# Performance work log

Measured on AMD Instinct MI355X. Metric: run time of the kernel, lower is better.

## Reference

```python
import jax, jax.numpy as jnp
import numpy as np

EPS = 1e-7

# ---- Poincare ball (c=1) manifold ops ----

def _logmap0(y):
    n = jnp.linalg.norm(y, axis=-1, keepdims=True)
    n = jnp.clip(n, EPS, 1.0 - 1e-5)
    return jnp.arctanh(n) * y / n


def _expmap0(v):
    n = jnp.maximum(jnp.linalg.norm(v, axis=-1, keepdims=True), EPS)
    return jnp.tanh(n) * v / n


def _pair_dist(q):
    # q: [B,N,H,D] points in the Poincare ball.
    # d(x,y) = arccosh(1 + 2||x-y||^2 / ((1-||x||^2)(1-||y||^2)))  (== 2 artanh ||(-x)+_m y||)
    sq = jnp.sum(q * q, axis=-1)                       # [B,N,H]
    dot = jnp.einsum('bnhd,bmhd->bnmh', q, q)          # [B,N,N,H] (batched GEMM)
    diff = jnp.maximum(sq[:, :, None, :] + sq[:, None, :, :] - 2.0 * dot, 0.0)
    denom = jnp.maximum((1.0 - sq[:, :, None, :]) * (1.0 - sq[:, None, :, :]), EPS)
    return jnp.arccosh(jnp.maximum(1.0 + 2.0 * diff / denom, 1.0 + EPS))  # [B,N,N,H]


def _hgat(x, adj, W, a_src, a_dst, multihead):
    # Hyperbolic GAT layer: log-map to tangent at origin, per-head linear +
    # masked GAT attention, exp-map back. use_act=False, no bias.
    xt = _logmap0(x)                                   # [B,N,Din]
    h = jnp.einsum('bnd,hde->bnhe', xt, W)             # [B,N,H,D]
    es = jnp.einsum('bnhe,he->bnh', h, a_src)
    ed = jnp.einsum('bnhe,he->bnh', h, a_dst)
    e = jax.nn.leaky_relu(es[:, :, None, :] + ed[:, None, :, :], 0.2)  # [B,N,N,H]
    e = jnp.where(adj[:, :, :, None] > 0, e, -1e9)
    att = jax.nn.softmax(e, axis=2)                    # over neighbors
    out = jnp.einsum('bnmh,bmhe->bnhe', att, h)        # [B,N,H,D]
    if multihead:
        return _expmap0(out)                           # per-head hyperbolic points
    B, N, H, D = out.shape
    return _expmap0(out.reshape(B, N, H * D))          # concat heads


def setup_inputs() -> dict:
    key = jax.random.key(0)
    B, N, DIN, DATT, DOUT, H = 8, 1024, 256, 64, 256, 4
    ks = jax.random.split(key, 8)
    x = _expmap0(0.5 * jax.random.normal(ks[0], (B, N, DIN), dtype=jnp.float32))
    a0 = (jax.random.uniform(ks[1], (B, N, N)) < 0.05).astype(jnp.float32)
    adj = jnp.maximum(a0, jnp.swapaxes(a0, -1, -2))
    adj = jnp.maximum(adj, jnp.eye(N, dtype=jnp.float32)[None])
    flags = jnp.ones((B, N), dtype=jnp.float32)
    s_in = 1.0 / np.sqrt(DIN)
    Wq = jax.random.normal(ks[2], (H, DIN, DATT), dtype=jnp.float32) * s_in
    aq_src = jax.random.normal(ks[3], (H, DATT), dtype=jnp.float32) / np.sqrt(DATT)
    aq_dst = jax.random.normal(ks[4], (H, DATT), dtype=jnp.float32) / np.sqrt(DATT)
    Dv = DOUT // H
    Wv = jax.random.normal(ks[5], (H, DIN, Dv), dtype=jnp.float32) * s_in
    av_src = jax.random.normal(ks[6], (H, Dv), dtype=jnp.float32) / np.sqrt(Dv)
    av_dst = jax.random.normal(ks[7], (H, Dv), dtype=jnp.float32) / np.sqrt(Dv)
    r = jnp.ones((H,), dtype=jnp.float32) * 5.0
    t = jnp.ones((H,), dtype=jnp.float32)
    return {"x": x, "adj": adj, "flags": flags, "Wq": Wq, "aq_src": aq_src,
            "aq_dst": aq_dst, "Wv": Wv, "av_src": av_src, "av_dst": av_dst,
            "r": r, "t": t}


def reference(x, adj, flags, Wq, aq_src, aq_dst, Wv, av_src, av_dst, r, t):
    B, N = adj.shape[0], adj.shape[1]
    query = _hgat(x, adj, Wq, aq_src, aq_dst, True)    # [B,N,H,DATT]
    value = _hgat(x, adj, Wv, av_src, av_dst, False)   # [B,N,DOUT]
    dist = _pair_dist(query)                           # [B,N,N,H]
    dist = dist.reshape(-1, B, N, N)                   # faithful torch .view(-1,*adj.shape)
    att = jnp.tanh((r[:, None, None, None] - dist) * t[:, None, None, None])
    att = att.reshape(-1, B, N, N).mean(axis=0)        # head-average -> [B,N,N]
    att = (att + jnp.swapaxes(att, -1, -2)) / 2.0      # symmetrize
    return value, att
```

## Files before the change

### kernel.cpp

```cpp
#include <hip/hip_runtime.h>
#include <hip/hip_bf16.h>
#include <math.h>

#define DEV __device__ __forceinline__

constexpr int B = 8, N = 1024, DIN = 256, H = 4, DATT = 64, DV = 64;
constexpr int BN = B * N;
constexpr int HD = H * DATT;
constexpr int HDV = H * DV;
constexpr int COLS = HD + HDV;
constexpr int BHN = B * H * N;
constexpr float EPSF = 1e-7f;

using short8 = __attribute__((ext_vector_type(8))) short;
using f32x4  = __attribute__((ext_vector_type(4))) float;

DEV unsigned short f2bf(float f) {
    __hip_bfloat16 h = __float2bfloat16(f);
    return *reinterpret_cast<unsigned short*>(&h);
}
DEV float bfu2f(unsigned short u) { return __uint_as_float(((unsigned)u) << 16); }

__global__ void k_scale(const float* __restrict__ x, float* __restrict__ s) {
    int p = blockIdx.x * 4 + (threadIdx.x >> 6);
    int l = threadIdx.x & 63;
    const float4* xr = reinterpret_cast<const float4*>(x + (size_t)p * DIN);
    float4 u = xr[l];
    float ss = u.x * u.x + u.y * u.y + u.z * u.z + u.w * u.w;
    for (int m = 32; m; m >>= 1) ss += __shfl_xor(ss, m);
    if (l == 0) {
        float n = sqrtf(ss);
        n = fminf(fmaxf(n, EPSF), 1.0f - 1e-5f);
        float at = 0.5f * __logf((1.f + n) / (1.f - n));
        s[p] = at / n;
    }
}

__global__ void k_wcat(const float* __restrict__ Wq, const float* __restrict__ Wv,
                       float* __restrict__ Wc) {
    int idx = blockIdx.x * 256 + threadIdx.x;
    int k = idx >> 9, c = idx & 511;
    int cc = c & 255;
    int h = cc >> 6, e = cc & 63;
    const float* src = (c < HD) ? Wq : Wv;
    Wc[idx] = src[(h * DIN + k) * 64 + e];
}

__global__ __launch_bounds__(256) void k_gemm(const float* __restrict__ x,
                                              const float* __restrict__ s,
                                              const float* __restrict__ Wc,
                                              float* __restrict__ hall) {
    __shared__ float As[16][68];
    __shared__ float Bs[16][68];
    int bm = blockIdx.x, bn = blockIdx.y;
    int tid = threadIdx.x;
    int ty = tid >> 4, tx = tid & 15;
    float acc[4][4] = {};
    int rowbase = bm * 64, colbase = bn * 64;
    int am = tid >> 2;
    int ak = (tid & 3) * 4;
    float sc = s[rowbase + am];
    for (int kt = 0; kt < DIN; kt += 16) {
        float4 u = *reinterpret_cast<const float4*>(x + (size_t)(rowbase + am) * DIN + kt + ak);
        As[ak + 0][am] = u.x * sc;
        As[ak + 1][am] = u.y * sc;
        As[ak + 2][am] = u.z * sc;
        As[ak + 3][am] = u.w * sc;
        int bk = tid >> 4, bc = (tid & 15) * 4;
        float4 w4 = *reinterpret_cast<const float4*>(Wc + (size_t)(kt + bk) * COLS + colbase + bc);
        *reinterpret_cast<float4*>(&Bs[bk][bc]) = w4;
        __syncthreads();
        for (int k = 0; k < 16; k++) {
            float4 a4 = *reinterpret_cast<const float4*>(&As[k][ty * 4]);
            float4 b4 = *reinterpret_cast<const float4*>(&Bs[k][tx * 4]);
            float av[4] = {a4.x, a4.y, a4.z, a4.w};
            float bv[4] = {b4.x, b4.y, b4.z, b4.w};
            for (int i = 0; i < 4; i++)
                for (int j = 0; j < 4; j++) acc[i][j] = fmaf(av[i], bv[j], acc[i][j]);
        }
        __syncthreads();
    }
    for (int i = 0; i < 4; i++) {
        float4 o = make_float4(acc[i][0], acc[i][1], acc[i][2], acc[i][3]);
        *reinterpret_cast<float4*>(hall + (size_t)(rowbase + ty * 4 + i) * COLS + colbase + tx * 4) = o;
    }
}

__global__ __launch_bounds__(256) void k_hT(const float* __restrict__ hall,
                                            unsigned short* __restrict__ hallT) {
    int jt = blockIdx.x, h = blockIdx.y, b = blockIdx.z;
    __shared__ float T[64][69];
    int t = threadIdx.x;
    int bh = b * H + h;
    int jl = t >> 2, cg = t & 3;
    int el = t >> 2, seg = t & 3;
    #pragma unroll
    for (int pass = 0; pass < 2; pass++) {
        int colbase = (pass == 0) ? h * 64 : 256 + h * 64;
        __syncthreads();
        {
            const float* src = hall + (size_t)(b * N + jt * 64 + jl) * COLS + colbase + cg * 16;
            #pragma unroll
            for (int u = 0; u < 4; u++) {
                float4 v = *reinterpret_cast<const float4*>(src + u * 4);
                T[jl][cg * 16 + u * 4 + 0] = v.x;
                T[jl][cg * 16 + u * 4 + 1] = v.y;
                T[jl][cg * 16 + u * 4 + 2] = v.z;
                T[jl][cg * 16 + u * 4 + 3] = v.w;
            }
        }
        __syncthreads();
        {
            unsigned int pk[8];
            #pragma unroll
            for (int k = 0; k < 8; k++) {
                float f0 = T[seg * 16 + 2 * k][el];
                float f1 = T[seg * 16 + 2 * k + 1][el];
                pk[k] = (unsigned)f2bf(f0) | ((unsigned)f2bf(f1) << 16);
            }
            unsigned short* dst = hallT + ((size_t)(bh * 128 + pass * 64 + el)) * 1024
                                  + jt * 64 + seg * 16;
            *reinterpret_cast<uint4*>(dst)     = make_uint4(pk[0], pk[1], pk[2], pk[3]);
            *reinterpret_cast<uint4*>(dst + 8) = make_uint4(pk[4], pk[5], pk[6], pk[7]);
        }
    }
}

__global__ void k_esed(const float* __restrict__ hall, const float* __restrict__ aqs,
                       const float* __restrict__ aqd, const float* __restrict__ avs,
                       const float* __restrict__ avd, float* __restrict__ esq,
                       float* __restrict__ edq, float* __restrict__ esv,
                       float* __restrict__ edv) {
    int p = blockIdx.x;
    int h = threadIdx.x >> 6, e = threadIdx.x & 63;
    float hq = hall[(size_t)p * COLS + h * 64 + e];
    float hv = hall[(size_t)p * COLS + 256 + h * 64 + e];
    float v1 = hq * aqs[h * 64 + e];
    float v2 = hq * aqd[h * 64 + e];
    float v3 = hv * avs[h * 64 + e];
    float v4 = hv * avd[h * 64 + e];
    for (int m = 32; m; m >>= 1) {
        v1 += __shfl_xor(v1, m); v2 += __shfl_xor(v2, m);
        v3 += __shfl_xor(v3, m); v4 += __shfl_xor(v4, m);
    }
    if (e == 0) {
        int b = p >> 10, n = p & 1023;
        int o = (b * H + h) * N + n;
        esq[o] = v1; edq[o] = v2; esv[o] = v3; edv[o] = v4;
    }
}

__global__ void k_stats(const float* __restrict__ adj, const float* __restrict__ esq,
                        const float* __restrict__ edq, const float* __restrict__ esv,
                        const float* __restrict__ edv, float* __restrict__ stats) {
    int bid = blockIdx.x;
    int i = bid & 1023;
    int bh = bid >> 10;
    int b = bh >> 2;
    int t = threadIdx.x;
    float esqi = esq[bid], esvi = esv[bid];
    const float* arow = adj + (size_t)(b * N + i) * N + t * 8;
    const float* edqr = edq + (size_t)bh * N + t * 8;
    const float* edvr = edv + (size_t)bh * N + t * 8;
    float4 a0 = *reinterpret_cast<const float4*>(arow);
    float4 a1 = *reinterpret_cast<const float4*>(arow + 4);
    float am[8] = {a0.x, a0.y, a0.z, a0.w, a1.x, a1.y, a1.z, a1.w};
    float4 q0 = *reinterpret_cast<const float4*>(edqr);
    float4 q1 = *reinterpret_cast<const float4*>(edqr + 4);
    float4 w0 = *reinterpret_cast<const float4*>(edvr);
    float4 w1 = *reinterpret_cast<const float4*>(edvr + 4);
    float edqv[8] = {q0.x, q0.y, q0.z, q0.w, q1.x, q1.y, q1.z, q1.w};
    float edvv[8] = {w0.x, w0.y, w0.z, w0.w, w1.x, w1.y, w1.z, w1.w};
    float eq[8], ev[8];
    float mq = -1e30f, mv = -1e30f;
    for (int j = 0; j < 8; j++) {
        bool msk = am[j] > 0.f;
        float q = esqi + edqv[j]; q = fmaxf(q, 0.2f * q);
        float v = esvi + edvv[j]; v = fmaxf(v, 0.2f * v);
        eq[j] = msk ? q : -1e30f;
        ev[j] = msk ? v : -1e30f;
        mq = fmaxf(mq, eq[j]); mv = fmaxf(mv, ev[j]);
    }
    __shared__ float red[2][2];
    __shared__ float red2[2][2];
    for (int m = 32; m; m >>= 1) { mq = fmaxf(mq, __shfl_xor(mq, m)); mv = fmaxf(mv, __shfl_xor(mv, m)); }
    int w = t >> 6;
    if ((t & 63) == 0) { red[w][0] = mq; red[w][1] = mv; }
    __syncthreads();
    mq = fmaxf(red[0][0], red[1][0]);
    mv = fmaxf(red[0][1], red[1][1]);
    float sq_ = 0.f, sv_ = 0.f;
    for (int j = 0; j < 8; j++) { sq_ += __expf(eq[j] - mq); sv_ += __expf(ev[j] - mv); }
    for (int m = 32; m; m >>= 1) { sq_ += __shfl_xor(sq_, m); sv_ += __shfl_xor(sv_, m); }
    if ((t & 63) == 0) { red2[w][0] = sq_; red2[w][1] = sv_; }
    __syncthreads();
    if (t == 0) {
        stats[bid] = mq;
        stats[BHN + bid] = red2[0][0] + red2[1][0];
        stats[2 * BHN + bid] = mv;
        stats[3 * BHN + bid] = red2[0][1] + red2[1][1];
    }
}

__global__ __launch_bounds__(512) void k_aggr(const float* __restrict__ adj,
        const unsigned short* __restrict__ hallT, const float* __restrict__ esq,
        const float* __restrict__ edq, const float* __restrict__ esv,
        const float* __restrict__ edv, const float* __restrict__ stats,
        float* __restrict__ outq, float* __restrict__ outv) {
    int f = blockIdx.x;
    int g = ((f & 7) << 7) | (f >> 3);
    int it = g & 31;
    int bh = g >> 5;
    int h = bh & 3, b = bh >> 2;
    int i0 = it * 32;
    int t = threadIdx.x;
    int lane = t & 63, wv = t >> 6;
    int team = wv >> 1;
    int mh = wv & 1;

    int i = i0 + mh * 16 + (lane & 15);
    int bi = bh * N + i;
    float esq_i = esq[bi], esv_i = esv[bi];
    float mq_i = stats[bi];           float isq_i = 1.f / stats[BHN + bi];
    float mv_i = stats[2 * BHN + bi]; float isv_i = 1.f / stats[3 * BHN + bi];
    const float* adjrow = adj + (size_t)(b * N + i) * N;
    const float* edqrow = edq + (size_t)bh * N;
    const float* edvrow = edv + (size_t)bh * N;
    int klo = lane >> 4;
    const unsigned short* bbq = hallT
        + ((size_t)(bh * 128 + (lane & 15))) * 1024 + klo * 8;
    const unsigned short* bbv = bbq + (size_t)64 * 1024;

    f32x4 accq[4] = {}, accv[4] = {};
    int jbase = team * 256;
    for (int jj = 0; jj < 8; jj++) {
        int j0 = jbase + jj * 32;
        float4 a0 = *reinterpret_cast<const float4*>(adjrow + j0 + klo * 8);
        float4 a1 = *reinterpret_cast<const float4*>(adjrow + j0 + klo * 8 + 4);
        float4 q0 = *reinterpret_cast<const float4*>(edqrow + j0 + klo * 8);
        float4 q1 = *reinterpret_cast<const float4*>(edqrow + j0 + klo * 8 + 4);
        float4 v0 = *reinterpret_cast<const float4*>(edvrow + j0 + klo * 8);
        float4 v1 = *reinterpret_cast<const float4*>(edvrow + j0 + klo * 8 + 4);
        float av[8] = {a0.x, a0.y, a0.z, a0.w, a1.x, a1.y, a1.z, a1.w};
        float eq[8] = {q0.x, q0.y, q0.z, q0.w, q1.x, q1.y, q1.z, q1.w};
        float ev[8] = {v0.x, v0.y, v0.z, v0.w, v1.x, v1.y, v1.z, v1.w};
        short8 afq, afv;
        #pragma unroll
        for (int u = 0; u < 8; u++) {
            bool on = av[u] > 0.f;
            float q = esq_i + eq[u]; q = fmaxf(q, 0.2f * q);
            float v = esv_i + ev[u]; v = fmaxf(v, 0.2f * v);
            float wq = on ? __expf(q - mq_i) * isq_i : 0.f;
            float wvv = on ? __expf(v - mv_i) * isv_i : 0.f;
            afq[u] = (short)f2bf(wq);
            afv[u] = (short)f2bf(wvv);
        }
        #pragma unroll
        for (int nt = 0; nt < 4; nt++) {
            short8 bq = *reinterpret_cast<const short8*>(bbq + j0 + nt * 16384);
            accq[nt] = __builtin_amdgcn_mfma_f32_16x16x32_bf16(afq, bq, accq[nt], 0, 0, 0);
            short8 bv = *reinterpret_cast<const short8*>(bbv + j0 + nt * 16384);
            accv[nt] = __builtin_amdgcn_mfma_f32_16x16x32_bf16(afv, bv, accv[nt], 0, 0, 0);
        }
    }

    __shared__ __align__(16) float red[8192];
    int slot = (team >> 1) * 2 + mh;
    float* buf = red + slot * 2048;
    __syncthreads();
    if (team & 1) {
        #pragma unroll
        for (int k = 0; k < 4; k++) {
            *reinterpret_cast<f32x4*>(&buf[(k * 64 + lane) * 4])       = accq[k];
            *reinterpret_cast<f32x4*>(&buf[((k + 4) * 64 + lane) * 4]) = accv[k];
        }
    }
    __syncthreads();
    if (!(team & 1)) {
        #pragma unroll
        for (int k = 0; k < 4; k++) {
            f32x4 pq = *reinterpret_cast<const f32x4*>(&buf[(k * 64 + lane) * 4]);
            f32x4 pv = *reinterpret_cast<const f32x4*>(&buf[((k + 4) * 64 + lane) * 4]);
            accq[k] += pq; accv[k] += pv;
        }
    }
    __syncthreads();
    if (team == 2) {
        float* d2 = red + mh * 2048;
        #pragma unroll
        for (int k = 0; k < 4; k++) {
            *reinterpret_cast<f32x4*>(&d2[(k * 64 + lane) * 4])       = accq[k];
            *reinterpret_cast<f32x4*>(&d2[((k + 4) * 64 + lane) * 4]) = accv[k];
        }
    }
    __syncthreads();
    if (team == 0) {
        float* s2 = red + mh * 2048;
        #pragma unroll
        for (int nt = 0; nt < 4; nt++) {
            f32x4 pq = *reinterpret_cast<const f32x4*>(&s2[(nt * 64 + lane) * 4]);
            f32x4 pv = *reinterpret_cast<const f32x4*>(&s2[((nt + 4) * 64 + lane) * 4]);
            #pragma unroll
            for (int r = 0; r < 4; r++) {
                int irow = i0 + mh * 16 + (lane >> 4) * 4 + r;
                int e = nt * 16 + (lane & 15);
                outq[(size_t)(b * N + irow) * 256 + h * 64 + e] = accq[nt][r] + pq[r];
                outv[(size_t)(b * N + irow) * 256 + h * 64 + e] = accv[nt][r] + pv[r];
            }
        }
    }
}

__global__ void k_expmap(const float* __restrict__ outq, const float* __restrict__ outv,
                         float* __restrict__ query, float* __restrict__ sq,
                         float* __restrict__ val) {
    int p = blockIdx.x, t = threadIdx.x;
    int h = t >> 6, e = t & 63;
    float v = outq[(size_t)p * HD + t];
    float ss = v * v;
    for (int m = 32; m; m >>= 1) ss += __shfl_xor(ss, m);
    float n = fmaxf(sqrtf(ss), EPSF);
    float tn = tanhf(n);
    query[(size_t)p * HD + t] = v * (tn / n);
    if (e == 0) sq[h * BN + p] = tn * tn;

    float vv = outv[(size_t)p * HDV + t];
    float s2 = vv * vv;
    for (int m = 32; m; m >>= 1) s2 += __shfl_xor(s2, m);
    __shared__ float part[4];
    if (e == 0) part[h] = s2;
    __syncthreads();
    float tot = part[0] + part[1] + part[2] + part[3];
    float nv = fmaxf(sqrtf(tot), EPSF);
    float sclv = tanhf(nv) / nv;
    val[(size_t)p * HDV + t] = vv * sclv;
}

DEV int swzX(int row, int ch) { return row * 64 + ((ch ^ (row & 7)) * 8); }

DEV void tsplit(float v, short& hs, short& ls) {
    unsigned vu = __float_as_uint(v);
    float lo = v - __uint_as_float(vu & 0xFFFF0000u);
    hs = (short)(unsigned short)(vu >> 16);
    ls = (short)(unsigned short)(__float_as_uint(lo) >> 16);
}

__global__ __launch_bounds__(256, 3) void k_att(const float* __restrict__ query,
        const float* __restrict__ sq, const float* __restrict__ rr,
        const float* __restrict__ tt, float* __restrict__ m_out) {
    int kc = blockIdx.x >> 1, xh = blockIdx.x & 1;
    int c = blockIdx.y >> 2, h = blockIdx.y & 3;
    int b2 = blockIdx.z;
    int t = threadIdx.x;
    int l = t & 63, w = t >> 6;

    __shared__ __align__(16) unsigned short Xh[64 * 64], Xl[64 * 64];
    __shared__ __align__(16) unsigned short Yh[128 * 64], Yl[128 * 64];
    __shared__ float sqX[64], sqY[128], isX[64], isY[128];

    int nstart = (b2 * 256 + kc * 64) & 1023;
    int mstart = c * 256 + xh * 128;

    int rowX = t >> 2, pX = t & 3;
    int rowY = t >> 1, pY = t & 1;

    float tacc[8][4] = {};

    #pragma unroll
    for (int a = 0; a < 4; a++) {
        int b = 2 * a + (b2 >> 2);
        __syncthreads();
        {
            const float4* sx4 = reinterpret_cast<const float4*>(
                query + (size_t)(b * N + nstart + rowX) * HD + h * 64);
            #pragma unroll
            for (int cch = 0; cch < 2; cch++) {
                short8 hx, lx;
                float4 v0 = sx4[pX * 4 + cch * 2];
                float4 v1 = sx4[pX * 4 + cch * 2 + 1];
                float vv[8] = {v0.x, v0.y, v0.z, v0.w, v1.x, v1.y, v1.z, v1.w};
                #pragma unroll
                for (int q = 0; q < 8; q++) { short hs, ls; tsplit(vv[q], hs, ls); hx[q] = hs; lx[q] = ls; }
                int idx = swzX(rowX, pX * 2 + cch);
                *reinterpret_cast<short8*>(&Xh[idx]) = hx;
                *reinterpret_cast<short8*>(&Xl[idx]) = lx;
            }
        }
        {
            const float4* sy4 = reinterpret_cast<const float4*>(
                query + (size_t)(b * N + mstart + rowY) * HD + h * 64);
            #pragma unroll
            for (int cch = 0; cch < 4; cch++) {
                short8 hy, ly;
                float4 v0 = sy4[pY * 8 + cch * 2];
                float4 v1 = sy4[pY * 8 + cch * 2 + 1];
                float vv[8] = {v0.x, v0.y, v0.z, v0.w, v1.x, v1.y, v1.z, v1.w};
                #pragma unroll
                for (int q = 0; q < 8; q++) { short hs, ls; tsplit(vv[q], hs, ls); hy[q] = hs; ly[q] = ls; }
                int idy = swzX(rowY, pY * 4 + cch);
                *reinterpret_cast<short8*>(&Yh[idy]) = hy;
                *reinterpret_cast<short8*>(&Yl[idy]) = ly;
            }
        }
        if (t < 64)  { float s = sq[h * BN + b * N + nstart + t]; sqX[t] = s; isX[t] = __builtin_amdgcn_rcpf(1.f - s); }
        else if (t < 192) { int tt2 = t - 64; float s = sq[h * BN + b * N + mstart + tt2]; sqY[tt2] = s; isY[tt2] = __builtin_amdgcn_rcpf(1.f - s); }
        __syncthreads();

        short8 Ah[2], Al[2];
        #pragma unroll
        for (int kk = 0; kk < 2; kk++) {
            int rx = w * 16 + (l & 15);
            int idx = swzX(rx, kk * 4 + (l >> 4));
            Ah[kk] = *reinterpret_cast<const short8*>(&Xh[idx]);
            Al[kk] = *reinterpret_cast<const short8*>(&Xl[idx]);
        }
        float ra = rr[a], ta = tt[a];
        float c1 = 2.f * ta;
        float c0 = c1 * ra * 1.44269504f;
        float sxr[4], ixr[4];
        #pragma unroll
        for (int r = 0; r < 4; r++) {
            int rx = w * 16 + (l >> 4) * 4 + r;
            sxr[r] = sqX[rx];
            ixr[r] = 2.f * isX[rx];
        }
        #pragma unroll
        for (int nt = 0; nt < 8; nt++) {
            int ry = nt * 16 + (l & 15);
            f32x4 acc = {};
            #pragma unroll
            for (int kk = 0; kk < 2; kk++) {
                int idy = swzX(ry, kk * 4 + (l >> 4));
                short8 Bh = *reinterpret_cast<const short8*>(&Yh[idy]);
                short8 Bl = *reinterpret_cast<const short8*>(&Yl[idy]);
                acc = __builtin_amdgcn_mfma_f32_16x16x32_bf16(Ah[kk], Bh, acc, 0, 0, 0);
                acc = __builtin_amdgcn_mfma_f32_16x16x32_bf16(Ah[kk], Bl, acc, 0, 0, 0);
                acc = __builtin_amdgcn_mfma_f32_16x16x32_bf16(Al[kk], Bh, acc, 0, 0, 0);
            }
            float sy = sqY[ry];
            float iy = isY[ry];
            #pragma unroll
            for (int r = 0; r < 4; r++) {
                float diff = fmaxf(fmaf(-2.f, acc[r], sxr[r] + sy), 0.f);
                float ixy = fminf(ixr[r] * iy, 2e7f);
                float z = fmaxf(fmaf(diff, ixy, 1.f), 1.f + EPSF);
                float s_ = z + __builtin_amdgcn_sqrtf(fmaf(z, z, -1.f));
                float l2 = __builtin_amdgcn_logf(s_);
                float ex = __builtin_amdgcn_exp2f(fmaf(-c1, l2, c0));
                float rc = __builtin_amdgcn_rcpf(ex + 1.f);
                tacc[nt][r] += fmaf(-2.f, rc, 1.f);
            }
        }
    }
    #pragma unroll
    for (int nt = 0; nt < 8; nt++) {
        #pragma unroll
        for (int r = 0; r < 4; r++) {
            int n_local = w * 16 + (l >> 4) * 4 + r;
            int n2 = c + 4 * (kc * 64 + n_local);
            int mloc = xh * 128 + nt * 16 + (l & 15);
            int m2 = 4 * mloc + h;
            m_out[((size_t)b2 << 20) + ((size_t)n2 << 10) + m2] = 0.25f * tacc[nt][r];
        }
    }
}

__global__ void k_sym(float* __restrict__ m) {
    int ti = blockIdx.x, tj = blockIdx.y, b = blockIdx.z;
    if (ti > tj) return;
    __shared__ float A[32][33], Bt[32][33];
    int t = threadIdx.x;
    int r = t >> 3, c4 = (t & 7) * 4;
    size_t baseA = ((size_t)b << 20) + (size_t)(ti * 32) * N + tj * 32;
    size_t baseB = ((size_t)b << 20) + (size_t)(tj * 32) * N + ti * 32;
    float4 ua = *reinterpret_cast<const float4*>(m + baseA + (size_t)r * N + c4);
    float4 ub = *reinterpret_cast<const float4*>(m + baseB + (size_t)r * N + c4);
    A[r][c4 + 0] = ua.x; A[r][c4 + 1] = ua.y; A[r][c4 + 2] = ua.z; A[r][c4 + 3] = ua.w;
    Bt[r][c4 + 0] = ub.x; Bt[r][c4 + 1] = ub.y; Bt[r][c4 + 2] = ub.z; Bt[r][c4 + 3] = ub.w;
    __syncthreads();
    for (int u = 0; u < 4; u++) {
        int cc = c4 + u;
        float oa = 0.5f * (A[r][cc] + Bt[cc][r]);
        float ob = 0.5f * (Bt[r][cc] + A[cc][r]);
        m[baseA + (size_t)r * N + cc] = oa;
        m[baseB + (size_t)r * N + cc] = ob;
    }
}

extern "C" void kernel_launch(void* const* d_in, const int* in_sizes, int n_in,
                              void* d_out, int out_size, void* d_ws, size_t ws_size,
                              hipStream_t stream) {
    const float* x   = (const float*)d_in[0];
    const float* adj = (const float*)d_in[1];
    const float* Wq  = (const float*)d_in[3];
    const float* aqs = (const float*)d_in[4];
    const float* aqd = (const float*)d_in[5];
    const float* Wv  = (const float*)d_in[6];
    const float* avs = (const float*)d_in[7];
    const float* avd = (const float*)d_in[8];
    const float* rr  = (const float*)d_in[9];
    const float* tt  = (const float*)d_in[10];

    float* ws = (float*)d_ws;
    float* s     = ws;
    float* Wc    = s + BN;
    float* hall  = Wc + 256 * COLS;
    float* esq   = hall + (size_t)BN * COLS;
    float* edq   = esq + BHN;
    float* esv   = edq + BHN;
    float* edv   = esv + BHN;
    float* stats = edv + BHN;
    float* outq  = stats + 4 * BHN;
    float* outv  = outq + (size_t)BN * HD;
    float* query = outq;
    float* sq    = outv + (size_t)BN * HDV;
    unsigned short* hallT = (unsigned short*)(sq + H * BN);
    size_t need = (size_t)((char*)(hallT + (size_t)BN * COLS) - (char*)ws);
    if (ws_size < need) return;

    float* val  = (float*)d_out;
    float* matt = (float*)d_out + (size_t)BN * HDV;

    k_scale<<<BN / 4, 256, 0, stream>>>(x, s);
    k_wcat<<<(256 * COLS) / 256, 256, 0, stream>>>(Wq, Wv, Wc);
    k_gemm<<<dim3(BN / 64, COLS / 64), 256, 0, stream>>>(x, s, Wc, hall);
    k_hT<<<dim3(16, H, B), 256, 0, stream>>>(hall, hallT);
    k_esed<<<BN, 256, 0, stream>>>(hall, aqs, aqd, avs, avd, esq, edq, esv, edv);
    k_stats<<<BHN, 128, 0, stream>>>(adj, esq, edq, esv, edv, stats);
    k_aggr<<<1024, 512, 0, stream>>>(adj, hallT, esq, edq, esv, edv, stats, outq, outv);
    k_expmap<<<BN, 256, 0, stream>>>(outq, outv, query, sq, val);
    k_att<<<dim3(8, 16, 8), 256, 0, stream>>>(query, sq, rr, tt, matt);
    k_sym<<<dim3(32, 32, 8), 256, 0, stream>>>(matt);
}
```

Measured before the change: 265.5 us.

## Precompute bf16 hi/lo query split in expmap and load MFMA operands from global

k_expmap now writes the query as precomputed bf16 high/low halves plus the reciprocal 1/(1-|q|^2), reusing the hall workspace. k_att drops its shared-memory staging, per-tile splitting and barriers, and instead loads MFMA operand fragments and the norm terms straight from global memory (relying on L1/L2). Its grid is flattened to 1D with a remapped block order to improve cache locality, and the occupancy hint is removed. This cuts LDS traffic, sync and redundant conversion work, but it adds uncoalesced, repeated global loads inside the inner loop.

```diff
diff --git a/kernel.cpp b/kernel.cpp
--- a/kernel.cpp
+++ b/kernel.cpp
@@ -20,6 +20,13 @@
     return *reinterpret_cast<unsigned short*>(&h);
 }
 DEV float bfu2f(unsigned short u) { return __uint_as_float(((unsigned)u) << 16); }
+
+DEV void tsplit(float v, short& hs, short& ls) {
+    unsigned vu = __float_as_uint(v);
+    float lo = v - __uint_as_float(vu & 0xFFFF0000u);
+    hs = (short)(unsigned short)(vu >> 16);
+    ls = (short)(unsigned short)(__float_as_uint(lo) >> 16);
+}
 
 __global__ void k_scale(const float* __restrict__ x, float* __restrict__ s) {
     int p = blockIdx.x * 4 + (threadIdx.x >> 6);
@@ -312,7 +319,8 @@
 }
 
 __global__ void k_expmap(const float* __restrict__ outq, const float* __restrict__ outv,
-                         float* __restrict__ query, float* __restrict__ sq,
+                         unsigned short* __restrict__ qh, unsigned short* __restrict__ ql,
+                         float* __restrict__ sq, float* __restrict__ isr,
                          float* __restrict__ val) {
     int p = blockIdx.x, t = threadIdx.x;
     int h = t >> 6, e = t & 63;
@@ -321,8 +329,15 @@
     for (int m = 32; m; m >>= 1) ss += __shfl_xor(ss, m);
     float n = fmaxf(sqrtf(ss), EPSF);
     float tn = tanhf(n);
-    query[(size_t)p * HD + t] = v * (tn / n);
-    if (e == 0) sq[h * BN + p] = tn * tn;
+    float qv = v * (tn / n);
+    short hs, ls; tsplit(qv, hs, ls);
+    qh[((size_t)p << 8) + t] = (unsigned short)hs;
+    ql[((size_t)p << 8) + t] = (unsigned short)ls;
+    if (e == 0) {
+        float s = tn * tn;
+        sq[h * BN + p] = s;
+        isr[h * BN + p] = __builtin_amdgcn_rcpf(1.f - s);
+    }
 
     float vv = outv[(size_t)p * HDV + t];
     float s2 = vv * vv;
@@ -336,83 +351,33 @@
     val[(size_t)p * HDV + t] = vv * sclv;
 }
 
-DEV int swzX(int row, int ch) { return row * 64 + ((ch ^ (row & 7)) * 8); }
-
-DEV void tsplit(float v, short& hs, short& ls) {
-    unsigned vu = __float_as_uint(v);
-    float lo = v - __uint_as_float(vu & 0xFFFF0000u);
-    hs = (short)(unsigned short)(vu >> 16);
-    ls = (short)(unsigned short)(__float_as_uint(lo) >> 16);
-}
-
-__global__ __launch_bounds__(256, 3) void k_att(const float* __restrict__ query,
-        const float* __restrict__ sq, const float* __restrict__ rr,
+__global__ __launch_bounds__(256) void k_att(const unsigned short* __restrict__ qh,
+        const unsigned short* __restrict__ ql, const float* __restrict__ sq,
+        const float* __restrict__ isr, const float* __restrict__ rr,
         const float* __restrict__ tt, float* __restrict__ m_out) {
-    int kc = blockIdx.x >> 1, xh = blockIdx.x & 1;
-    int c = blockIdx.y >> 2, h = blockIdx.y & 3;
-    int b2 = blockIdx.z;
+    int f = blockIdx.x;
+    int g = ((f & 7) << 7) | (f >> 3);
+    int b2 = g >> 7;
+    int rem = g & 127;
+    int c = rem >> 5, h = (rem >> 3) & 3, kc = (rem >> 1) & 3, xh = rem & 1;
     int t = threadIdx.x;
     int l = t & 63, w = t >> 6;
-
-    __shared__ __align__(16) unsigned short Xh[64 * 64], Xl[64 * 64];
-    __shared__ __align__(16) unsigned short Yh[128 * 64], Yl[128 * 64];
-    __shared__ float sqX[64], sqY[128], isX[64], isY[128];
+    int klo = l >> 4;
 
     int nstart = (b2 * 256 + kc * 64) & 1023;
     int mstart = c * 256 + xh * 128;
-
-    int rowX = t >> 2, pX = t & 3;
-    int rowY = t >> 1, pY = t & 1;
 
     float tacc[8][4] = {};
 
     #pragma unroll
     for (int a = 0; a < 4; a++) {
         int b = 2 * a + (b2 >> 2);
-        __syncthreads();
-        {
-            const float4* sx4 = reinterpret_cast<const float4*>(
-                query + (size_t)(b * N + nstart + rowX) * HD + h * 64);
-            #pragma unroll
-            for (int cch = 0; cch < 2; cch++) {
-                short8 hx, lx;
-                float4 v0 = sx4[pX * 4 + cch * 2];
-                float4 v1 = sx4[pX * 4 + cch * 2 + 1];
-                float vv[8] = {v0.x, v0.y, v0.z, v0.w, v1.x, v1.y, v1.z, v1.w};
-                #pragma unroll
-                for (int q = 0; q < 8; q++) { short hs, ls; tsplit(vv[q], hs, ls); hx[q] = hs; lx[q] = ls; }
-                int idx = swzX(rowX, pX * 2 + cch);
-                *reinterpret_cast<short8*>(&Xh[idx]) = hx;
-                *reinterpret_cast<short8*>(&Xl[idx]) = lx;
-            }
-        }
-        {
-            const float4* sy4 = reinterpret_cast<const float4*>(
-                query + (size_t)(b * N + mstart + rowY) * HD + h * 64);
-            #pragma unroll
-            for (int cch = 0; cch < 4; cch++) {
-                short8 hy, ly;
-                float4 v0 = sy4[pY * 8 + cch * 2];
-                float4 v1 = sy4[pY * 8 + cch * 2 + 1];
-                float vv[8] = {v0.x, v0.y, v0.z, v0.w, v1.x, v1.y, v1.z, v1.w};
-                #pragma unroll
-                for (int q = 0; q < 8; q++) { short hs, ls; tsplit(vv[q], hs, ls); hy[q] = hs; ly[q] = ls; }
-                int idy = swzX(rowY, pY * 4 + cch);
-                *reinterpret_cast<short8*>(&Yh[idy]) = hy;
-                *reinterpret_cast<short8*>(&Yl[idy]) = ly;
-            }
-        }
-        if (t < 64)  { float s = sq[h * BN + b * N + nstart + t]; sqX[t] = s; isX[t] = __builtin_amdgcn_rcpf(1.f - s); }
-        else if (t < 192) { int tt2 = t - 64; float s = sq[h * BN + b * N + mstart + tt2]; sqY[tt2] = s; isY[tt2] = __builtin_amdgcn_rcpf(1.f - s); }
-        __syncthreads();
-
+        size_t xbase = ((size_t)(b * N + nstart + w * 16 + (l & 15)) << 8) + h * 64 + klo * 8;
         short8 Ah[2], Al[2];
         #pragma unroll
         for (int kk = 0; kk < 2; kk++) {
-            int rx = w * 16 + (l & 15);
-            int idx = swzX(rx, kk * 4 + (l >> 4));
-            Ah[kk] = *reinterpret_cast<const short8*>(&Xh[idx]);
-            Al[kk] = *reinterpret_cast<const short8*>(&Xl[idx]);
+            Ah[kk] = *reinterpret_cast<const short8*>(qh + xbase + kk * 32);
+            Al[kk] = *reinterpret_cast<const short8*>(ql + xbase + kk * 32);
         }
         float ra = rr[a], ta = tt[a];
         float c1 = 2.f * ta;
@@ -420,25 +385,26 @@
         float sxr[4], ixr[4];
         #pragma unroll
         for (int r = 0; r < 4; r++) {
-            int rx = w * 16 + (l >> 4) * 4 + r;
-            sxr[r] = sqX[rx];
-            ixr[r] = 2.f * isX[rx];
-        }
+            int gx = h * BN + b * N + nstart + w * 16 + (l >> 4) * 4 + r;
+            sxr[r] = sq[gx];
+            ixr[r] = 2.f * isr[gx];
+        }
+        size_t ybase = ((size_t)(b * N + mstart + (l & 15)) << 8) + h * 64 + klo * 8;
         #pragma unroll
         for (int nt = 0; nt < 8; nt++) {
-            int ry = nt * 16 + (l & 15);
+            size_t yb = ybase + ((size_t)(nt * 16) << 8);
             f32x4 acc = {};
             #pragma unroll
             for (int kk = 0; kk < 2; kk++) {
-                int idy = swzX(ry, kk * 4 + (l >> 4));
-                short8 Bh = *reinterpret_cast<const short8*>(&Yh[idy]);
-                short8 Bl = *reinterpret_cast<const short8*>(&Yl[idy]);
+                short8 Bh = *reinterpret_cast<const short8*>(qh + yb + kk * 32);
+                short8 Bl = *reinterpret_cast<const short8*>(ql + yb + kk * 32);
                 acc = __builtin_amdgcn_mfma_f32_16x16x32_bf16(Ah[kk], Bh, acc, 0, 0, 0);
                 acc = __builtin_amdgcn_mfma_f32_16x16x32_bf16(Ah[kk], Bl, acc, 0, 0, 0);
                 acc = __builtin_amdgcn_mfma_f32_16x16x32_bf16(Al[kk], Bh, acc, 0, 0, 0);
             }
-            float sy = sqY[ry];
-            float iy = isY[ry];
+            int gy = h * BN + b * N + mstart + nt * 16 + (l & 15);
+            float sy = sq[gy];
+            float iy = isr[gy];
             #pragma unroll
             for (int r = 0; r < 4; r++) {
                 float diff = fmaxf(fmaf(-2.f, acc[r], sxr[r] + sy), 0.f);
@@ -512,11 +478,14 @@
     float* stats = edv + BHN;
     float* outq  = stats + 4 * BHN;
     float* outv  = outq + (size_t)BN * HD;
-    float* query = outq;
     float* sq    = outv + (size_t)BN * HDV;
     unsigned short* hallT = (unsigned short*)(sq + H * BN);
     size_t need = (size_t)((char*)(hallT + (size_t)BN * COLS) - (char*)ws);
     if (ws_size < need) return;
+
+    unsigned short* qh = (unsigned short*)hall;
+    unsigned short* ql = qh + (size_t)BN * 256;
+    float* isr = (float*)(ql + (size_t)BN * 256);
 
     float* val  = (float*)d_out;
     float* matt = (float*)d_out + (size_t)BN * HDV;
@@ -528,7 +497,7 @@
     k_esed<<<BN, 256, 0, stream>>>(hall, aqs, aqd, avs, avd, esq, edq, esv, edv);
     k_stats<<<BHN, 128, 0, stream>>>(adj, esq, edq, esv, edv, stats);
     k_aggr<<<1024, 512, 0, stream>>>(adj, hallT, esq, edq, esv, edv, stats, outq, outv);
-    k_expmap<<<BN, 256, 0, stream>>>(outq, outv, query, sq, val);
-    k_att<<<dim3(8, 16, 8), 256, 0, stream>>>(query, sq, rr, tt, matt);
+    k_expmap<<<BN, 256, 0, stream>>>(outq, outv, qh, ql, sq, isr, val);
+    k_att<<<1024, 256, 0, stream>>>(qh, ql, sq, isr, rr, tt, matt);
     k_sym<<<dim3(32, 32, 8), 256, 0, stream>>>(matt);
 }
```

Result: no change. 263.0 us (-0.9%).
